# Kernel tuning notes

Measured on AMD Instinct MI355X. Metric: run time of the kernel, lower is better.

The kernel has to match this reference:

```python
import jax, jax.numpy as jnp
import numpy as np

B, S, D = 16, 1024, 768          # batch, seq_len, in_features
NS, MAXW = 256, 8                # num_spans, max span width (fixed for jit)
V, C = 128, 6                    # num_vertexes, max corefs per vertex
R = 512                          # num_max_rels_per_example
REL, HID, DIS = 97, 384, 20      # relation_num, hidden_dim, dis_size
NEG = -1e30


def setup_inputs() -> dict:
    key = jax.random.key(0)
    ks = jax.random.split(key, 14)
    sentence_repr = jax.random.normal(ks[0], (B, S, D), jnp.float32)
    starts = jax.random.randint(ks[1], (B, NS), 0, S - MAXW)
    widths = jax.random.randint(ks[2], (B, NS), 0, MAXW)
    entity_span_indices = jnp.stack([starts, starts + widths], axis=-1)  # (B,NS,2), start<=end
    entity_span_indices_mask = jax.random.randint(ks[3], (B, NS), 0, 2)
    vertex_indices = jax.random.randint(ks[4], (B, V, C), 0, NS)
    vertex_indices_mask = jax.random.randint(ks[5], (B, V, C), 0, 2)
    head_tail_indices = jax.random.randint(ks[6], (B, R, 2), 0, V)
    relation_mask = jax.random.randint(ks[7], (B, R), 0, 2)
    dis_h_2_t = jax.random.randint(ks[8], (B, R), 0, 20)
    dis_t_2_h = jax.random.randint(ks[9], (B, R), 0, 20)
    dis_embed = jax.random.normal(ks[10], (20, DIS), jnp.float32) * 0.02
    dis_embed = dis_embed.at[10].set(0.0)  # padding_idx=10
    fin = D + DIS                      # final_in_features with distance
    in_proj = 2 * fin + D              # concat [head+dis, tail+dis, head*tail]
    W1 = jax.random.normal(ks[11], (in_proj, HID), jnp.float32) / np.float32(np.sqrt(in_proj))
    W2 = jax.random.normal(ks[12], (HID, REL), jnp.float32) / np.float32(np.sqrt(HID))
    b2 = jnp.zeros((REL,), jnp.float32)
    return dict(sentence_repr=sentence_repr, entity_span_indices=entity_span_indices,
                entity_span_indices_mask=entity_span_indices_mask,
                vertex_indices=vertex_indices, vertex_indices_mask=vertex_indices_mask,
                head_tail_indices=head_tail_indices, relation_mask=relation_mask,
                dis_h_2_t=dis_h_2_t, dis_t_2_h=dis_t_2_h,
                dis_embed=dis_embed, W1=W1, W2=W2, b2=b2)


def reference(sentence_repr, entity_span_indices, entity_span_indices_mask,
              vertex_indices, vertex_indices_mask, head_tail_indices,
              relation_mask, dis_h_2_t, dis_t_2_h, dis_embed, W1, W2, b2):
    Bx, Sx, Dx = sentence_repr.shape
    # --- SpanExtractor: masked max pooling over tokens in each span [start, end] ---
    starts = entity_span_indices[..., 0]
    ends = entity_span_indices[..., 1]
    pos = starts[..., None] + jnp.arange(MAXW)            # (B,NS,W)
    valid = pos <= ends[..., None]
    posc = jnp.clip(pos, 0, Sx - 1).reshape(Bx, -1)       # (B,NS*W)
    tok = jnp.take_along_axis(sentence_repr, posc[..., None], axis=1)
    tok = tok.reshape(Bx, NS, MAXW, Dx)
    span_emb = jnp.where(valid[..., None], tok, NEG).max(axis=2)   # (B,NS,D)
    # --- coref 'mean' pooling over spans per vertex (batched_index_select) ---
    vidx = vertex_indices.reshape(Bx, -1)
    ve = jnp.take_along_axis(span_emb, vidx[..., None], axis=1).reshape(Bx, V, C, Dx)
    m = vertex_indices_mask.astype(jnp.float32)
    cnt = jnp.maximum(m.sum(axis=2), 1.0)                 # num_corefs clamped >=1
    vertex_emb = (ve * m[..., None]).sum(axis=2) / cnt[..., None]  # (B,V,D)
    # --- head/tail gather ---
    hti = head_tail_indices.reshape(Bx, -1)
    ht = jnp.take_along_axis(vertex_emb, hti[..., None], axis=1).reshape(Bx, R, 2, Dx)
    head_repr = ht[:, :, 0, :]
    tail_repr = ht[:, :, 1, :]
    # (original multiplies by relation_mask and discards the result -> no-op)
    eh = dis_embed[dis_h_2_t]                              # (B,R,DIS)
    et = dis_embed[dis_t_2_h]
    feat = jnp.concatenate([head_repr, eh, tail_repr, et, head_repr * tail_repr], axis=-1)
    # TwoLayerLinear: relu(x @ W1) @ W2 + b2, bias=(False, True)
    predict_re = jax.nn.relu(feat @ W1) @ W2 + b2          # (B,R,REL)
    return predict_re
```

## Files before the change

### kernel.cpp

```cpp
#include <hip/hip_runtime.h>
#include <cstdint>
#include <cstddef>

#define B_    16
#define S_    1024
#define D_    768
#define NS_   256
#define V_    128
#define C_    6
#define R_    512
#define REL_  97
#define HID_  384
#define DIS_  20
#define K1_   2344
#define KP_   2368
#define N2P_  128

typedef unsigned short ushort_t;
typedef short bf16x8 __attribute__((ext_vector_type(8)));
typedef float f32x4  __attribute__((ext_vector_type(4)));

__device__ __forceinline__ float bf2f(short s) {
    return __uint_as_float(((unsigned int)(unsigned short)s) << 16);
}
__device__ __forceinline__ short f2bf(float x) {
    union { float f; unsigned int u; } c; c.f = x;
    unsigned int r = (c.u + 0x7fffu + ((c.u >> 16) & 1u)) >> 16;
    return (short)(unsigned short)r;
}

__global__ __launch_bounds__(256) void span_kernel(
    const float* __restrict__ sr, const int* __restrict__ spans,
    float* __restrict__ span_emb)
{
    int bn    = blockIdx.x;
    int b     = bn >> 8;
    int start = spans[2 * bn];
    int end   = spans[2 * bn + 1];
    int w     = end - start;
    const float* base = sr + ((size_t)b * S_ + start) * D_;
    float* out = span_emb + (size_t)bn * D_;
    int tid = threadIdx.x;
#pragma unroll
    for (int e = 0; e < 3; ++e) {
        int d = tid + e * 256;
        float m = base[d];
        for (int j = 1; j <= w; ++j) m = fmaxf(m, base[(size_t)j * D_ + d]);
        out[d] = m;
    }
}

__global__ __launch_bounds__(256) void vertex_kernel(
    const float* __restrict__ span_emb, const int* __restrict__ vidx,
    const int* __restrict__ vmask, ushort_t* __restrict__ vembB)
{
    int bv = blockIdx.x;
    int b  = bv >> 7;
    const int* vi = vidx  + bv * C_;
    const int* vm = vmask + bv * C_;
    int   idxs[C_];
    float ms[C_];
    float cnt = 0.f;
#pragma unroll
    for (int c = 0; c < C_; ++c) {
        idxs[c] = vi[c];
        ms[c]   = (float)vm[c];
        cnt    += ms[c];
    }
    float inv = 1.f / fmaxf(cnt, 1.f);
    int tid = threadIdx.x;
    ushort_t* out = vembB + (size_t)bv * D_;
#pragma unroll
    for (int e = 0; e < 3; ++e) {
        int d = tid + e * 256;
        float s = 0.f;
#pragma unroll
        for (int c = 0; c < C_; ++c) {
            if (ms[c] != 0.f)
                s += span_emb[((size_t)(b * NS_ + idxs[c])) * D_ + d];
        }
        out[d] = (ushort_t)f2bf(s * inv);
    }
}

__global__ __launch_bounds__(384) void wconv_kernel(
    const float* __restrict__ W1, const float* __restrict__ W2,
    ushort_t* __restrict__ W1T, ushort_t* __restrict__ W2T)
{
    int tid = threadIdx.x;
    if (blockIdx.x < 148) {
        int k0 = blockIdx.x * 16;
        int n  = tid;
#pragma unroll
        for (int i = 0; i < 16; ++i) {
            int k = k0 + i;
            int orig;
            if      (k < 768)  orig = k;
            else if (k < 1536) orig = k + 20;
            else if (k < 2304) orig = k + 40;
            else if (k < 2324) orig = 768 + (k - 2304);
            else if (k < K1_)  orig = 1556 + (k - 2324);
            else               orig = -1;
            float v = (orig >= 0) ? W1[(size_t)orig * HID_ + n] : 0.f;
            W1T[(size_t)n * KP_ + k] = (ushort_t)f2bf(v);
        }
    } else {
        int bid = blockIdx.x - 148;
#pragma unroll
        for (int i = 0; i < 16; ++i) {
            int e = bid * 6144 + tid + i * 384;
            int n = e / HID_;
            int k = e - n * HID_;
            float v = (n < REL_) ? W2[(size_t)k * REL_ + n] : 0.f;
            W2T[e] = (ushort_t)f2bf(v);
        }
    }
}

__global__ __launch_bounds__(256) void gemm1_kernel(
    const ushort_t* __restrict__ vembB, const int* __restrict__ ht,
    const int* __restrict__ dht, const int* __restrict__ dth,
    const float* __restrict__ dis, const ushort_t* __restrict__ W1T,
    ushort_t* __restrict__ hiddenB)
{
    __shared__ ushort_t As[64][72];
    __shared__ ushort_t Bs[64][72];

    int m0  = blockIdx.x * 64;
    int n0  = blockIdx.y * 64;
    int tid = threadIdx.x;

    int arow0 = tid >> 3;
    int akk   = (tid & 7) * 8;

    int g0 = m0 + arow0, g1 = g0 + 32;
    int b0 = g0 >> 9,    b1 = g1 >> 9;
    int rh0 = b0 * V_ + ht[2 * g0], rt0 = b0 * V_ + ht[2 * g0 + 1];
    int rh1 = b1 * V_ + ht[2 * g1], rt1 = b1 * V_ + ht[2 * g1 + 1];
    int rdh0 = dht[g0], rdt0 = dth[g0];
    int rdh1 = dht[g1], rdt1 = dth[g1];

    auto stageA = [&](int kk0, int rh_, int rt_, int rdh_, int rdt_) -> bf16x8 {
        int kg = kk0 + akk;
        if (kk0 < 768) {
            return *(const bf16x8*)(vembB + (size_t)rh_ * D_ + kg);
        } else if (kk0 < 1536) {
            return *(const bf16x8*)(vembB + (size_t)rt_ * D_ + (kg - 768));
        } else if (kk0 < 2304) {
            int kd = kg - 1536;
            bf16x8 h = *(const bf16x8*)(vembB + (size_t)rh_ * D_ + kd);
            bf16x8 t = *(const bf16x8*)(vembB + (size_t)rt_ * D_ + kd);
            bf16x8 p;
#pragma unroll
            for (int j = 0; j < 8; ++j) p[j] = f2bf(bf2f(h[j]) * bf2f(t[j]));
            return p;
        } else {
            bf16x8 p;
#pragma unroll
            for (int j = 0; j < 8; ++j) {
                int kglob = kg + j;
                float v = 0.f;
                if      (kglob < 2324) v = dis[rdh_ * DIS_ + (kglob - 2304)];
                else if (kglob < K1_)  v = dis[rdt_ * DIS_ + (kglob - 2324)];
                p[j] = f2bf(v);
            }
            return p;
        }
    };

    bf16x8 pA0, pA1, pB0, pB1;
    auto loadAB = [&](int kk0) {
        pA0 = stageA(kk0, rh0, rt0, rdh0, rdt0);
        pA1 = stageA(kk0, rh1, rt1, rdh1, rdt1);
        pB0 = *(const bf16x8*)(W1T + (size_t)(n0 + arow0)      * KP_ + kk0 + akk);
        pB1 = *(const bf16x8*)(W1T + (size_t)(n0 + arow0 + 32) * KP_ + kk0 + akk);
    };

    int w    = tid >> 6;
    int lane = tid & 63;
    int wm = (w & 1) * 32, wn = (w >> 1) * 32;
    int lr = lane & 15, lq = lane >> 4;

    f32x4 acc00 = {0.f, 0.f, 0.f, 0.f};
    f32x4 acc01 = acc00, acc10 = acc00, acc11 = acc00;

    loadAB(0);
    for (int k0 = 0; k0 < KP_; k0 += 64) {
        __syncthreads();
        *(bf16x8*)&As[arow0][akk]      = pA0;
        *(bf16x8*)&As[arow0 + 32][akk] = pA1;
        *(bf16x8*)&Bs[arow0][akk]      = pB0;
        *(bf16x8*)&Bs[arow0 + 32][akk] = pB1;
        __syncthreads();
        if (k0 + 64 < KP_) loadAB(k0 + 64);
#pragma unroll
        for (int ks = 0; ks < 2; ++ks) {
            int kb = ks * 32 + lq * 8;
            bf16x8 a0 = *(bf16x8*)&As[wm + lr][kb];
            bf16x8 a1 = *(bf16x8*)&As[wm + 16 + lr][kb];
            bf16x8 bb0 = *(bf16x8*)&Bs[wn + lr][kb];
            bf16x8 bb1 = *(bf16x8*)&Bs[wn + 16 + lr][kb];
            acc00 = __builtin_amdgcn_mfma_f32_16x16x32_bf16(a0, bb0, acc00, 0, 0, 0);
            acc01 = __builtin_amdgcn_mfma_f32_16x16x32_bf16(a0, bb1, acc01, 0, 0, 0);
            acc10 = __builtin_amdgcn_mfma_f32_16x16x32_bf16(a1, bb0, acc10, 0, 0, 0);
            acc11 = __builtin_amdgcn_mfma_f32_16x16x32_bf16(a1, bb1, acc11, 0, 0, 0);
        }
    }

    int grow = m0 + wm + lq * 4;
    int gcol = n0 + wn + lr;
    auto st = [&](f32x4 v, int rr, int cc) {
#pragma unroll
        for (int r = 0; r < 4; ++r)
            hiddenB[(size_t)(rr + r) * HID_ + cc] =
                (ushort_t)f2bf(fmaxf(v[r], 0.f));
    };
    st(acc00, grow,      gcol);
    st(acc01, grow,      gcol + 16);
    st(acc10, grow + 16, gcol);
    st(acc11, grow + 16, gcol + 16);
}

__global__ __launch_bounds__(256) void gemm2_kernel(
    const ushort_t* __restrict__ hiddenB, const ushort_t* __restrict__ W2T,
    const float* __restrict__ b2, float* __restrict__ out)
{
    __shared__ ushort_t As[32][72];
    __shared__ ushort_t Bs[128][72];

    int m0  = blockIdx.x * 32;
    int tid = threadIdx.x;

    int arow = tid >> 3;
    int akk  = (tid & 7) * 8;

    bf16x8 pA, pB[4];
    auto loadAB = [&](int k0) {
        pA = *(const bf16x8*)(hiddenB + (size_t)(m0 + arow) * HID_ + k0 + akk);
#pragma unroll
        for (int e = 0; e < 4; ++e)
            pB[e] = *(const bf16x8*)(W2T + (size_t)(arow + e * 32) * HID_ + k0 + akk);
    };

    int w    = tid >> 6;
    int lane = tid & 63;
    int wm = (w & 1) * 16;
    int wn = (w >> 1) * 64;
    int lr = lane & 15, lq = lane >> 4;

    f32x4 acc[4];
#pragma unroll
    for (int e = 0; e < 4; ++e) acc[e] = (f32x4){0.f, 0.f, 0.f, 0.f};

    loadAB(0);
    for (int k0 = 0; k0 < HID_; k0 += 64) {
        __syncthreads();
        *(bf16x8*)&As[arow][akk] = pA;
#pragma unroll
        for (int e = 0; e < 4; ++e)
            *(bf16x8*)&Bs[arow + e * 32][akk] = pB[e];
        __syncthreads();
        if (k0 + 64 < HID_) loadAB(k0 + 64);
#pragma unroll
        for (int ks = 0; ks < 2; ++ks) {
            int kb = ks * 32 + lq * 8;
            bf16x8 a = *(bf16x8*)&As[wm + lr][kb];
#pragma unroll
            for (int nf = 0; nf < 4; ++nf) {
                bf16x8 bb = *(bf16x8*)&Bs[wn + nf * 16 + lr][kb];
                acc[nf] = __builtin_amdgcn_mfma_f32_16x16x32_bf16(a, bb, acc[nf], 0, 0, 0);
            }
        }
    }

    int grow = m0 + wm + lq * 4;
#pragma unroll
    for (int nf = 0; nf < 4; ++nf) {
        int col = wn + nf * 16 + lr;
        if (col < REL_) {
            float bias = b2[col];
#pragma unroll
            for (int r = 0; r < 4; ++r)
                out[(size_t)(grow + r) * REL_ + col] = acc[nf][r] + bias;
        }
    }
}

extern "C" void kernel_launch(void* const* d_in, const int* in_sizes, int n_in,
                              void* d_out, int out_size, void* d_ws, size_t ws_size,
                              hipStream_t stream)
{
    const float* sr    = (const float*)d_in[0];
    const int*   spans = (const int*)  d_in[1];
    const int*   vidx  = (const int*)  d_in[3];
    const int*   vmask = (const int*)  d_in[4];
    const int*   ht    = (const int*)  d_in[5];
    const int*   dht   = (const int*)  d_in[7];
    const int*   dth   = (const int*)  d_in[8];
    const float* dis   = (const float*)d_in[9];
    const float* W1    = (const float*)d_in[10];
    const float* W2    = (const float*)d_in[11];
    const float* b2    = (const float*)d_in[12];
    float* out = (float*)d_out;

    float*    span_emb = (float*)d_ws;
    ushort_t* vembB    = (ushort_t*)(span_emb + (size_t)B_ * NS_ * D_);
    ushort_t* W1T      = vembB + (size_t)B_ * V_ * D_;
    ushort_t* W2T      = W1T + (size_t)HID_ * KP_;
    ushort_t* hiddenB  = W2T + (size_t)N2P_ * HID_;

    span_kernel<<<B_ * NS_, 256, 0, stream>>>(sr, spans, span_emb);
    vertex_kernel<<<B_ * V_, 256, 0, stream>>>(span_emb, vidx, vmask, vembB);
    wconv_kernel<<<156, 384, 0, stream>>>(W1, W2, W1T, W2T);

    dim3 g1((B_ * R_) / 64, HID_ / 64);
    gemm1_kernel<<<g1, 256, 0, stream>>>(vembB, ht, dht, dth, dis, W1T, hiddenB);

    gemm2_kernel<<<(B_ * R_) / 32, 256, 0, stream>>>(hiddenB, W2T, b2, out);
}
```

Before: 177.6 us.

## Restructure gemm1 with 256x64 tiles, split-K atomics, LDS DMA and 32x32 MFMA

Rewrites the first GEMM to use 256x64 block tiles, 32x32x16 MFMA instructions and double-buffered LDS filled by direct global-to-LDS loads for the plain head, tail and weight segments. K is split four ways across blockIdx.z, and partial sums are accumulated into an fp32 hidden buffer with atomicAdd after a memset. ReLU and the bf16 conversion move into gemm2's load path. The goal is more data reuse per tile and better fill of the GPU. The cost is extra fp32 atomic traffic, a memset, a larger intermediate buffer, and split-K summation order that is not deterministic.

```diff
diff --git a/kernel.cpp b/kernel.cpp
--- a/kernel.cpp
+++ b/kernel.cpp
@@ -16,9 +16,14 @@
 #define KP_   2368
 #define N2P_  128
 
+#define BM1   256
+#define BN1   64
+
 typedef unsigned short ushort_t;
+typedef unsigned int   u32;
 typedef short bf16x8 __attribute__((ext_vector_type(8)));
 typedef float f32x4  __attribute__((ext_vector_type(4)));
+typedef float f32x16 __attribute__((ext_vector_type(16)));
 
 __device__ __forceinline__ float bf2f(short s) {
     return __uint_as_float(((unsigned int)(unsigned short)s) << 16);
@@ -27,6 +32,12 @@
     union { float f; unsigned int u; } c; c.f = x;
     unsigned int r = (c.u + 0x7fffu + ((c.u >> 16) & 1u)) >> 16;
     return (short)(unsigned short)r;
+}
+
+typedef const __attribute__((address_space(1))) u32* gas_t;
+typedef __attribute__((address_space(3))) u32*       las_t;
+__device__ __forceinline__ void dma16(const void* g, void* l) {
+    __builtin_amdgcn_global_load_lds((gas_t)g, (las_t)l, 16, 0, 0);
 }
 
 __global__ __launch_bounds__(256) void span_kernel(
@@ -117,112 +128,120 @@
     }
 }
 
-__global__ __launch_bounds__(256) void gemm1_kernel(
+__global__ __launch_bounds__(256, 2) void gemm1_kernel(
     const ushort_t* __restrict__ vembB, const int* __restrict__ ht,
     const int* __restrict__ dht, const int* __restrict__ dth,
     const float* __restrict__ dis, const ushort_t* __restrict__ W1T,
-    ushort_t* __restrict__ hiddenB)
-{
-    __shared__ ushort_t As[64][72];
-    __shared__ ushort_t Bs[64][72];
-
-    int m0  = blockIdx.x * 64;
-    int n0  = blockIdx.y * 64;
-    int tid = threadIdx.x;
-
-    int arow0 = tid >> 3;
-    int akk   = (tid & 7) * 8;
-
-    int g0 = m0 + arow0, g1 = g0 + 32;
-    int b0 = g0 >> 9,    b1 = g1 >> 9;
-    int rh0 = b0 * V_ + ht[2 * g0], rt0 = b0 * V_ + ht[2 * g0 + 1];
-    int rh1 = b1 * V_ + ht[2 * g1], rt1 = b1 * V_ + ht[2 * g1 + 1];
-    int rdh0 = dht[g0], rdt0 = dth[g0];
-    int rdh1 = dht[g1], rdt1 = dth[g1];
-
-    auto stageA = [&](int kk0, int rh_, int rt_, int rdh_, int rdt_) -> bf16x8 {
-        int kg = kk0 + akk;
-        if (kk0 < 768) {
-            return *(const bf16x8*)(vembB + (size_t)rh_ * D_ + kg);
-        } else if (kk0 < 1536) {
-            return *(const bf16x8*)(vembB + (size_t)rt_ * D_ + (kg - 768));
-        } else if (kk0 < 2304) {
-            int kd = kg - 1536;
-            bf16x8 h = *(const bf16x8*)(vembB + (size_t)rh_ * D_ + kd);
-            bf16x8 t = *(const bf16x8*)(vembB + (size_t)rt_ * D_ + kd);
-            bf16x8 p;
-#pragma unroll
-            for (int j = 0; j < 8; ++j) p[j] = f2bf(bf2f(h[j]) * bf2f(t[j]));
-            return p;
+    float* __restrict__ hiddenF)
+{
+    __shared__ ushort_t Abuf[2][8][BM1][8];
+    __shared__ ushort_t Bbuf[2][8][BN1][8];
+
+    int tid  = threadIdx.x;
+    int wv   = tid >> 6;
+    int lane = tid & 63;
+    int m0   = blockIdx.x * BM1;
+    int n0   = blockIdx.y * BN1;
+    int ks   = blockIdx.z;
+    int it0  = (ks == 0) ? 0 : 10 + (ks - 1) * 9;
+    int itN  = (ks == 0) ? 10 : 9;
+
+    int srow = wv * 64 + lane;
+    int g    = m0 + srow;
+    int b    = g >> 9;
+    int rh   = b * V_ + ht[2 * g];
+    int rt   = b * V_ + ht[2 * g + 1];
+    const ushort_t* headp = vembB + (size_t)rh * D_;
+    const ushort_t* tailp = vembB + (size_t)rt * D_;
+    int rdh = dht[g], rdt = dth[g];
+    const ushort_t* bsrc = W1T + (size_t)(n0 + lane) * KP_;
+
+    auto stage = [&](int bf, int k0) {
+        int r    = k0 / 768;
+        int koff = k0 - r * 768;
+        if (r == 0) {
+#pragma unroll
+            for (int kg = 0; kg < 8; ++kg)
+                dma16(headp + koff + kg * 8, &Abuf[bf][kg][wv * 64][0]);
+        } else if (r == 1) {
+#pragma unroll
+            for (int kg = 0; kg < 8; ++kg)
+                dma16(tailp + koff + kg * 8, &Abuf[bf][kg][wv * 64][0]);
+        } else if (r == 2) {
+#pragma unroll
+            for (int kg = 0; kg < 8; ++kg) {
+                bf16x8 h = *(const bf16x8*)(headp + koff + kg * 8);
+                bf16x8 t = *(const bf16x8*)(tailp + koff + kg * 8);
+                bf16x8 p;
+#pragma unroll
+                for (int j = 0; j < 8; ++j) p[j] = f2bf(bf2f(h[j]) * bf2f(t[j]));
+                *(bf16x8*)&Abuf[bf][kg][srow][0] = p;
+            }
         } else {
-            bf16x8 p;
-#pragma unroll
-            for (int j = 0; j < 8; ++j) {
-                int kglob = kg + j;
-                float v = 0.f;
-                if      (kglob < 2324) v = dis[rdh_ * DIS_ + (kglob - 2304)];
-                else if (kglob < K1_)  v = dis[rdt_ * DIS_ + (kglob - 2324)];
-                p[j] = f2bf(v);
+#pragma unroll
+            for (int kg = 0; kg < 8; ++kg) {
+                bf16x8 p;
+#pragma unroll
+                for (int j = 0; j < 8; ++j) {
+                    int kk = kg * 8 + j;
+                    float v = 0.f;
+                    if      (kk < 20) v = dis[rdh * DIS_ + kk];
+                    else if (kk < 40) v = dis[rdt * DIS_ + (kk - 20)];
+                    p[j] = f2bf(v);
+                }
+                *(bf16x8*)&Abuf[bf][kg][srow][0] = p;
             }
-            return p;
-        }
+        }
+        dma16(bsrc + k0 + wv * 8,       &Bbuf[bf][wv][0][0]);
+        dma16(bsrc + k0 + (wv + 4) * 8, &Bbuf[bf][wv + 4][0][0]);
     };
 
-    bf16x8 pA0, pA1, pB0, pB1;
-    auto loadAB = [&](int kk0) {
-        pA0 = stageA(kk0, rh0, rt0, rdh0, rdt0);
-        pA1 = stageA(kk0, rh1, rt1, rdh1, rdt1);
-        pB0 = *(const bf16x8*)(W1T + (size_t)(n0 + arow0)      * KP_ + kk0 + akk);
-        pB1 = *(const bf16x8*)(W1T + (size_t)(n0 + arow0 + 32) * KP_ + kk0 + akk);
-    };
-
-    int w    = tid >> 6;
-    int lane = tid & 63;
-    int wm = (w & 1) * 32, wn = (w >> 1) * 32;
-    int lr = lane & 15, lq = lane >> 4;
-
-    f32x4 acc00 = {0.f, 0.f, 0.f, 0.f};
-    f32x4 acc01 = acc00, acc10 = acc00, acc11 = acc00;
-
-    loadAB(0);
-    for (int k0 = 0; k0 < KP_; k0 += 64) {
+    int half = lane >> 5;
+    int lrow = lane & 31;
+    int wm   = wv * 64;
+
+    f32x16 acc[2][2];
+#pragma unroll
+    for (int i = 0; i < 2; ++i)
+#pragma unroll
+        for (int j = 0; j < 2; ++j)
+#pragma unroll
+            for (int r = 0; r < 16; ++r) acc[i][j][r] = 0.f;
+
+    stage(0, it0 * 64);
+    for (int it = 0; it < itN; ++it) {
+        int bf = it & 1;
         __syncthreads();
-        *(bf16x8*)&As[arow0][akk]      = pA0;
-        *(bf16x8*)&As[arow0 + 32][akk] = pA1;
-        *(bf16x8*)&Bs[arow0][akk]      = pB0;
-        *(bf16x8*)&Bs[arow0 + 32][akk] = pB1;
-        __syncthreads();
-        if (k0 + 64 < KP_) loadAB(k0 + 64);
-#pragma unroll
-        for (int ks = 0; ks < 2; ++ks) {
-            int kb = ks * 32 + lq * 8;
-            bf16x8 a0 = *(bf16x8*)&As[wm + lr][kb];
-            bf16x8 a1 = *(bf16x8*)&As[wm + 16 + lr][kb];
-            bf16x8 bb0 = *(bf16x8*)&Bs[wn + lr][kb];
-            bf16x8 bb1 = *(bf16x8*)&Bs[wn + 16 + lr][kb];
-            acc00 = __builtin_amdgcn_mfma_f32_16x16x32_bf16(a0, bb0, acc00, 0, 0, 0);
-            acc01 = __builtin_amdgcn_mfma_f32_16x16x32_bf16(a0, bb1, acc01, 0, 0, 0);
-            acc10 = __builtin_amdgcn_mfma_f32_16x16x32_bf16(a1, bb0, acc10, 0, 0, 0);
-            acc11 = __builtin_amdgcn_mfma_f32_16x16x32_bf16(a1, bb1, acc11, 0, 0, 0);
-        }
-    }
-
-    int grow = m0 + wm + lq * 4;
-    int gcol = n0 + wn + lr;
-    auto st = [&](f32x4 v, int rr, int cc) {
-#pragma unroll
-        for (int r = 0; r < 4; ++r)
-            hiddenB[(size_t)(rr + r) * HID_ + cc] =
-                (ushort_t)f2bf(fmaxf(v[r], 0.f));
-    };
-    st(acc00, grow,      gcol);
-    st(acc01, grow,      gcol + 16);
-    st(acc10, grow + 16, gcol);
-    st(acc11, grow + 16, gcol + 16);
+        if (it + 1 < itN) stage(bf ^ 1, (it0 + it + 1) * 64);
+#pragma unroll
+        for (int s = 0; s < 4; ++s) {
+            int kg = s * 2 + half;
+            bf16x8 a0 = *(bf16x8*)&Abuf[bf][kg][wm + lrow][0];
+            bf16x8 a1 = *(bf16x8*)&Abuf[bf][kg][wm + 32 + lrow][0];
+            bf16x8 b0 = *(bf16x8*)&Bbuf[bf][kg][lrow][0];
+            bf16x8 b1 = *(bf16x8*)&Bbuf[bf][kg][32 + lrow][0];
+            acc[0][0] = __builtin_amdgcn_mfma_f32_32x32x16_bf16(a0, b0, acc[0][0], 0, 0, 0);
+            acc[0][1] = __builtin_amdgcn_mfma_f32_32x32x16_bf16(a0, b1, acc[0][1], 0, 0, 0);
+            acc[1][0] = __builtin_amdgcn_mfma_f32_32x32x16_bf16(a1, b0, acc[1][0], 0, 0, 0);
+            acc[1][1] = __builtin_amdgcn_mfma_f32_32x32x16_bf16(a1, b1, acc[1][1], 0, 0, 0);
+        }
+    }
+
+#pragma unroll
+    for (int fm = 0; fm < 2; ++fm)
+#pragma unroll
+        for (int fn = 0; fn < 2; ++fn) {
+            int col = n0 + fn * 32 + lrow;
+#pragma unroll
+            for (int r = 0; r < 16; ++r) {
+                int row = m0 + wm + fm * 32 + (r & 3) + 8 * (r >> 2) + 4 * half;
+                atomicAdd(hiddenF + (size_t)row * HID_ + col, acc[fm][fn][r]);
+            }
+        }
 }
 
 __global__ __launch_bounds__(256) void gemm2_kernel(
-    const ushort_t* __restrict__ hiddenB, const ushort_t* __restrict__ W2T,
+    const float* __restrict__ hiddenF, const ushort_t* __restrict__ W2T,
     const float* __restrict__ b2, float* __restrict__ out)
 {
     __shared__ ushort_t As[32][72];
@@ -234,9 +253,16 @@
     int arow = tid >> 3;
     int akk  = (tid & 7) * 8;
 
-    bf16x8 pA, pB[4];
+    bf16x8 pA; bf16x8 pB[4];
     auto loadAB = [&](int k0) {
-        pA = *(const bf16x8*)(hiddenB + (size_t)(m0 + arow) * HID_ + k0 + akk);
+        const float* hp = hiddenF + (size_t)(m0 + arow) * HID_ + k0 + akk;
+        f32x4 x = *(const f32x4*)hp;
+        f32x4 y = *(const f32x4*)(hp + 4);
+#pragma unroll
+        for (int j = 0; j < 4; ++j) {
+            pA[j]     = f2bf(fmaxf(x[j], 0.f));
+            pA[j + 4] = f2bf(fmaxf(y[j], 0.f));
+        }
 #pragma unroll
         for (int e = 0; e < 4; ++e)
             pB[e] = *(const bf16x8*)(W2T + (size_t)(arow + e * 32) * HID_ + k0 + akk);
@@ -307,14 +333,16 @@
     ushort_t* vembB    = (ushort_t*)(span_emb + (size_t)B_ * NS_ * D_);
     ushort_t* W1T      = vembB + (size_t)B_ * V_ * D_;
     ushort_t* W2T      = W1T + (size_t)HID_ * KP_;
-    ushort_t* hiddenB  = W2T + (size_t)N2P_ * HID_;
+    float*    hiddenF  = (float*)(W2T + (size_t)N2P_ * HID_);
+
+    hipMemsetAsync(hiddenF, 0, (size_t)B_ * R_ * HID_ * sizeof(float), stream);
 
     span_kernel<<<B_ * NS_, 256, 0, stream>>>(sr, spans, span_emb);
     vertex_kernel<<<B_ * V_, 256, 0, stream>>>(span_emb, vidx, vmask, vembB);
     wconv_kernel<<<156, 384, 0, stream>>>(W1, W2, W1T, W2T);
 
-    dim3 g1((B_ * R_) / 64, HID_ / 64);
-    gemm1_kernel<<<g1, 256, 0, stream>>>(vembB, ht, dht, dth, dis, W1T, hiddenB);
-
-    gemm2_kernel<<<(B_ * R_) / 32, 256, 0, stream>>>(hiddenB, W2T, b2, out);
-}
+    dim3 g1((B_ * R_) / BM1, HID_ / BN1, 4);
+    gemm1_kernel<<<g1, 256, 0, stream>>>(vembB, ht, dht, dth, dis, W1T, hiddenF);
+
+    gemm2_kernel<<<(B_ * R_) / 32, 256, 0, stream>>>(hiddenF, W2T, b2, out);
+}
```

New measurement: 219.4 us. 1.24x slower.
